# Kernel optimization log

Hardware: AMD Instinct MI355X
Metric: run time of the kernel (lower is better)

## Reference

```python
import jax, jax.numpy as jnp
import numpy as np

M = 8192      # nodes
D = 128       # feature dim
DEG = 32      # neighbors per node


def setup_inputs() -> dict:
    key = jax.random.key(0)
    ks = jax.random.split(key, 6)
    z = jax.random.normal(ks[0], (M, D), dtype=jnp.float32)
    # deterministic, duplicate-free edge list: node i -> (i+1..i+DEG) mod M
    src = jnp.repeat(jnp.arange(M, dtype=jnp.int64), DEG)
    dst = (src + jnp.tile(jnp.arange(1, DEG + 1, dtype=jnp.int64), M)) % M
    edge_index = jnp.stack([src, dst], axis=0)  # [2, M*DEG]
    s = 1.0 / np.sqrt(D)
    Wg = jax.random.normal(ks[1], (D, D), dtype=jnp.float32) * s
    Wc = jax.random.normal(ks[2], (D, D), dtype=jnp.float32) * s
    Wq = jax.random.normal(ks[3], (D, D), dtype=jnp.float32) * s
    Wk = jax.random.normal(ks[4], (D, D), dtype=jnp.float32) * s
    a = jax.random.normal(ks[5], (2 * D,), dtype=jnp.float32)
    return {"z": z, "edge_index": edge_index, "Wg": Wg, "Wc": Wc,
            "Wq": Wq, "Wk": Wk, "a": a}


def reference(z, edge_index, Wg, Wc, Wq, Wk, a):
    m, d = z.shape
    wg = z @ Wg.T                              # [m, d]
    src, dst = edge_index[0], edge_index[1]
    a_src, a_dst = a[:d], a[d:]
    # per-edge score: leaky_relu(a . [wg[i], wg[j]]) = leaky_relu(a1.wg[i] + a2.wg[j])
    scores = jax.nn.leaky_relu((wg @ a_src)[src] + (wg @ a_dst)[dst])  # [E]
    # softmax over each source node's neighbors (segment softmax)
    smax = jax.ops.segment_max(scores, src, num_segments=m)
    ex = jnp.exp(scores - smax[src])
    denom = jax.ops.segment_sum(ex, src, num_segments=m)
    alpha = ex / denom[src]                    # [E]
    # scatter-aggregate: local[i] = sum_j alpha_ij * wg[j]
    local = jax.ops.segment_sum(alpha[:, None] * wg[dst], src, num_segments=m)
    # dense global attention branch
    q = z @ Wq.T
    k = z @ Wk.T
    beta = jax.nn.softmax(q @ k.T / jnp.sqrt(jnp.float32(d)), axis=-1)  # [m, m]
    global_msg = beta @ (z @ Wc.T)
    return jax.nn.leaky_relu(local + global_msg + z)
```

## Files before the change

kernel.cpp:

```cpp
#include <hip/hip_runtime.h>

#define MM 8192
#define DD 128
#define DEG 32
#define KSPLIT 8
#define NB 16
#define RSTAGE 48

typedef __attribute__((ext_vector_type(8))) _Float16 h8;
typedef __attribute__((ext_vector_type(4))) float f4;
typedef __attribute__((ext_vector_type(4))) unsigned int u4;
typedef __attribute__((ext_vector_type(4))) short s4;

__device__ __forceinline__ unsigned short f2h(float f) {
  _Float16 h = (_Float16)f;
  return __builtin_bit_cast(unsigned short, h);
}

__device__ __forceinline__ void lds_dma16(const unsigned short* gptr, unsigned short* lptr) {
  __builtin_amdgcn_global_load_lds(
      (const __attribute__((address_space(1))) unsigned int*)gptr,
      (__attribute__((address_space(3))) unsigned int*)lptr, 16, 0, 0);
}

__global__ __launch_bounds__(256) void proj_kernel(
    const float* __restrict__ z, const float* __restrict__ Wg,
    const float* __restrict__ Wc, const float* __restrict__ Wq,
    const float* __restrict__ Wk, const float* __restrict__ a,
    float* __restrict__ wg, unsigned short* __restrict__ qb,
    unsigned short* __restrict__ kb, unsigned short* __restrict__ ct,
    float* __restrict__ sg, float* __restrict__ sd)
{
  __shared__ unsigned short zt[64 * 136];
  __shared__ unsigned short wt[128 * 136];
  const int mode = blockIdx.y;
  const float* __restrict__ W = (mode == 0) ? Wg : (mode == 1) ? Wq : (mode == 2) ? Wk : Wc;
  const int r0 = blockIdx.x * 64;
  const int tid = threadIdx.x;

  #pragma unroll
  for (int it = 0; it < 8; ++it) {
    int id = tid + it * 256, row = id >> 5, c4 = (id & 31) * 4;
    f4 v = *(const f4*)(z + (r0 + row) * DD + c4);
    s4 sv = {(short)f2h(v.x), (short)f2h(v.y), (short)f2h(v.z), (short)f2h(v.w)};
    *(s4*)&zt[row * 136 + c4] = sv;
  }
  #pragma unroll
  for (int it = 0; it < 16; ++it) {
    int id = tid + it * 256, row = id >> 5, c4 = (id & 31) * 4;
    f4 v = *(const f4*)(W + row * DD + c4);
    s4 sv = {(short)f2h(v.x), (short)f2h(v.y), (short)f2h(v.z), (short)f2h(v.w)};
    *(s4*)&wt[row * 136 + c4] = sv;
  }
  __syncthreads();

  const int lane = tid & 63, w = tid >> 6, n = lane & 15, quad = lane >> 4;
  h8 afr[4];
  #pragma unroll
  for (int kt = 0; kt < 4; ++kt)
    afr[kt] = *(const h8*)&zt[(16 * w + n) * 136 + kt * 32 + quad * 8];

  f4 acc[8];
  const f4 fzero = {0.f, 0.f, 0.f, 0.f};
  #pragma unroll
  for (int nt = 0; nt < 8; ++nt) {
    f4 c = fzero;
    #pragma unroll
    for (int kt = 0; kt < 4; ++kt) {
      h8 b = *(const h8*)&wt[(16 * nt + n) * 136 + kt * 32 + quad * 8];
      c = __builtin_amdgcn_mfma_f32_16x16x32_f16(afr[kt], b, c, 0, 0, 0);
    }
    acc[nt] = c;
  }

  if (mode == 0) {
    #pragma unroll
    for (int nt = 0; nt < 8; ++nt)
      #pragma unroll
      for (int r = 0; r < 4; ++r)
        wg[(r0 + 16 * w + quad * 4 + r) * DD + 16 * nt + n] = acc[nt][r];
    float av[8], bv[8];
    #pragma unroll
    for (int nt = 0; nt < 8; ++nt) { av[nt] = a[16 * nt + n]; bv[nt] = a[DD + 16 * nt + n]; }
    #pragma unroll
    for (int r = 0; r < 4; ++r) {
      float s1 = 0.f, s2 = 0.f;
      #pragma unroll
      for (int nt = 0; nt < 8; ++nt) { s1 += acc[nt][r] * av[nt]; s2 += acc[nt][r] * bv[nt]; }
      s1 += __shfl_xor(s1, 1); s1 += __shfl_xor(s1, 2); s1 += __shfl_xor(s1, 4); s1 += __shfl_xor(s1, 8);
      s2 += __shfl_xor(s2, 1); s2 += __shfl_xor(s2, 2); s2 += __shfl_xor(s2, 4); s2 += __shfl_xor(s2, 8);
      if (n == 0) {
        int g = r0 + 16 * w + quad * 4 + r;
        sg[g] = s1; sd[g] = s2;
      }
    }
  } else if (mode == 1) {
    const float qscale = 0.08838834764831845f;
    #pragma unroll
    for (int nt = 0; nt < 8; ++nt)
      #pragma unroll
      for (int r = 0; r < 4; ++r)
        qb[(r0 + 16 * w + quad * 4 + r) * DD + 16 * nt + n] = f2h(acc[nt][r] * qscale);
  } else if (mode == 2) {
    #pragma unroll
    for (int nt = 0; nt < 8; ++nt)
      #pragma unroll
      for (int r = 0; r < 4; ++r)
        kb[(r0 + 16 * w + quad * 4 + r) * DD + 16 * nt + n] = f2h(acc[nt][r]);
  } else {
    __syncthreads();
    #pragma unroll
    for (int nt = 0; nt < 8; ++nt)
      #pragma unroll
      for (int r = 0; r < 4; ++r)
        wt[(16 * nt + n) * 80 + 16 * w + quad * 4 + r] = f2h(acc[nt][r]);
    __syncthreads();
    #pragma unroll
    for (int it = 0; it < 4; ++it) {
      int idx = tid + it * 256, d = idx >> 3, c8 = (idx & 7) * 8;
      u4 v = *(const u4*)&wt[d * 80 + c8];
      *(u4*)(ct + (size_t)d * MM + r0 + c8) = v;
    }
  }
}

__global__ __launch_bounds__(256, 2) void flash_kernel(
    const unsigned short* __restrict__ qb, const unsigned short* __restrict__ kb,
    const unsigned short* __restrict__ ct, unsigned short* __restrict__ Opart,
    float* __restrict__ Lpart)
{
  __shared__ unsigned short sh[37376];
  const int bx = blockIdx.x, ck = blockIdx.y;
  const int tid = threadIdx.x, lane = tid & 63, w = tid >> 6;
  const int n = lane & 15, quad = lane >> 4;
  const int ln = n, lq = quad;
  const int qr0 = bx * 128;

  #pragma unroll
  for (int it = 0; it < 8; ++it)
    lds_dma16(qb + (qr0 + it * 16 + ln) * DD + w * 32 + lq * 8,
              &sh[(it * 256 + tid) * 8]);
  __syncthreads();
  h8 aq[2][4];
  #pragma unroll
  for (int mt = 0; mt < 2; ++mt)
    #pragma unroll
    for (int kt = 0; kt < 4; ++kt)
      aq[mt][kt] = *(const h8*)&sh[((w * 2 + mt) * 4 + kt) * 512 + lane * 8];
  __syncthreads();

  const unsigned short* kp = kb + (size_t)(ck * 1024 + 4 * ln) * DD + w * 32 + lq * 8;
  const unsigned short* vp = ct + (size_t)(16 * (w >> 1) + ln) * MM + ck * 1024 + (w & 1) * 32 + lq * 8;

  #pragma unroll
  for (int it = 0; it < 4; ++it)
    lds_dma16(kp + it * DD, &sh[(it * 256 + tid) * 8]);
  #pragma unroll
  for (int it = 0; it < 4; ++it)
    lds_dma16(vp + (size_t)it * 32 * MM, &sh[8192 + (it * 256 + tid) * 8]);

  f4 acc_o[2][8];
  const f4 fzero = {0.f, 0.f, 0.f, 0.f};
  #pragma unroll
  for (int mt = 0; mt < 2; ++mt)
    #pragma unroll
    for (int dt = 0; dt < 8; ++dt) acc_o[mt][dt] = fzero;
  float l_r[2][4] = {{0.f, 0.f, 0.f, 0.f}, {0.f, 0.f, 0.f, 0.f}};
  const int pbase = 32768 + w * 1152;

  for (int t = 0; t < 16; ++t) {
    __syncthreads();
    const int cur = (t & 1) * 16384;

    if (t < 15) {
      const int nb = ((t + 1) & 1) * 16384;
      const unsigned short* kpn = kp + (size_t)(t + 1) * 64 * DD;
      const unsigned short* vpn = vp + (t + 1) * 64;
      #pragma unroll
      for (int it = 0; it < 4; ++it)
        lds_dma16(kpn + it * DD, &sh[nb + (it * 256 + tid) * 8]);
      #pragma unroll
      for (int it = 0; it < 4; ++it)
        lds_dma16(vpn + (size_t)it * 32 * MM, &sh[nb + 8192 + (it * 256 + tid) * 8]);
    }

    f4 accs[2][4];
    #pragma unroll
    for (int mt = 0; mt < 2; ++mt)
      #pragma unroll
      for (int nt = 0; nt < 4; ++nt) accs[mt][nt] = fzero;
    #pragma unroll
    for (int nt = 0; nt < 4; ++nt) {
      #pragma unroll
      for (int kt = 0; kt < 4; ++kt) {
        h8 bk = *(const h8*)&sh[cur + nt * 2048 + kt * 512 + lane * 8];
        accs[0][nt] = __builtin_amdgcn_mfma_f32_16x16x32_f16(aq[0][kt], bk, accs[0][nt], 0, 0, 0);
        accs[1][nt] = __builtin_amdgcn_mfma_f32_16x16x32_f16(aq[1][kt], bk, accs[1][nt], 0, 0, 0);
      }
    }

    h8 ap[2][2];
    #pragma unroll
    for (int mt = 0; mt < 2; ++mt) {
      #pragma unroll
      for (int r = 0; r < 4; ++r) {
        float p0 = __expf(fminf(accs[mt][0][r], 10.f));
        float p1 = __expf(fminf(accs[mt][1][r], 10.f));
        float p2 = __expf(fminf(accs[mt][2][r], 10.f));
        float p3 = __expf(fminf(accs[mt][3][r], 10.f));
        l_r[mt][r] += p0 + p1 + p2 + p3;
        unsigned int lo = ((unsigned int)f2h(p1) << 16) | f2h(p0);
        unsigned int hi = ((unsigned int)f2h(p3) << 16) | f2h(p2);
        uint2 pv; pv.x = lo; pv.y = hi;
        *(uint2*)&sh[pbase + (quad * 4 + r) * 72 + n * 4] = pv;
      }
      ap[mt][0] = *(const h8*)&sh[pbase + n * 72 + quad * 8];
      ap[mt][1] = *(const h8*)&sh[pbase + n * 72 + 32 + quad * 8];
    }

    #pragma unroll
    for (int dt = 0; dt < 8; ++dt) {
      #pragma unroll
      for (int k2 = 0; k2 < 2; ++k2) {
        h8 bv = *(const h8*)&sh[cur + 8192 + dt * 1024 + k2 * 512 + lane * 8];
        acc_o[0][dt] = __builtin_amdgcn_mfma_f32_16x16x32_f16(ap[0][k2], bv, acc_o[0][dt], 0, 0, 0);
        acc_o[1][dt] = __builtin_amdgcn_mfma_f32_16x16x32_f16(ap[1][k2], bv, acc_o[1][dt], 0, 0, 0);
      }
    }
  }

  #pragma unroll
  for (int mt = 0; mt < 2; ++mt)
    #pragma unroll
    for (int r = 0; r < 4; ++r) {
      float lv = l_r[mt][r];
      lv += __shfl_xor(lv, 1); lv += __shfl_xor(lv, 2);
      lv += __shfl_xor(lv, 4); lv += __shfl_xor(lv, 8);
      int g = qr0 + w * 32 + mt * 16 + quad * 4 + r;
      if (n == 0) Lpart[ck * MM + g] = lv;
      #pragma unroll
      for (int dt = 0; dt < 8; ++dt)
        Opart[((size_t)ck * MM + g) * DD + 16 * dt + n] = f2h(acc_o[mt][dt][r]);
    }
}

__global__ __launch_bounds__(256) void merge_kernel(
    const int* __restrict__ ei, const float* __restrict__ wg,
    const float* __restrict__ sg, const float* __restrict__ sd,
    const unsigned short* __restrict__ Opart, const float* __restrict__ Lpart,
    const float* __restrict__ z, float* __restrict__ out)
{
  __shared__ float rows_s[RSTAGE * 132];
  __shared__ float sc_s[NB][DEG];
  __shared__ float alpha_s[NB][DEG];
  __shared__ int idx_s[NB][DEG];
  const int tid = threadIdx.x;
  const int i0 = blockIdx.x * NB;

  #pragma unroll
  for (int it = 0; it < 6; ++it) {
    int idx = tid + it * 256;
    int r = idx >> 5, c4 = (idx & 31) * 4;
    int grow = (i0 + 1 + r) & (MM - 1);
    *(f4*)&rows_s[r * 132 + c4] = *(const f4*)(wg + (size_t)grow * DD + c4);
  }
  #pragma unroll
  for (int it = 0; it < 2; ++it) {
    int e = tid + it * 256;
    int ni = e >> 5, j = e & 31;
    int i = i0 + ni;
    int dstj = ei[MM * DEG + i * DEG + j];
    float s = sg[i] + sd[dstj];
    sc_s[ni][j] = s > 0.f ? s : 0.01f * s;
    idx_s[ni][j] = (dstj - (i0 + 1)) & (MM - 1);
  }
  __syncthreads();

  if (tid < NB) {
    float mx = -1e30f;
    #pragma unroll 8
    for (int j = 0; j < DEG; ++j) mx = fmaxf(mx, sc_s[tid][j]);
    float sum = 0.f;
    #pragma unroll 8
    for (int j = 0; j < DEG; ++j) { float p = __expf(sc_s[tid][j] - mx); alpha_s[tid][j] = p; sum += p; }
    float inv = 1.f / sum;
    #pragma unroll 8
    for (int j = 0; j < DEG; ++j) alpha_s[tid][j] *= inv;
  }
  __syncthreads();

  const int ni = tid >> 4, d0 = (tid & 15) * 8;
  const int i = i0 + ni;
  float acc[8] = {0.f, 0.f, 0.f, 0.f, 0.f, 0.f, 0.f, 0.f};
  #pragma unroll 4
  for (int j = 0; j < DEG; ++j) {
    float al = alpha_s[ni][j];
    int r = idx_s[ni][j];
    if (r < RSTAGE) {
      const float* src = &rows_s[r * 132 + d0];
      #pragma unroll
      for (int q = 0; q < 8; ++q) acc[q] += al * src[q];
    } else {
      const float* src = wg + (size_t)((i0 + 1 + r) & (MM - 1)) * DD + d0;
      #pragma unroll
      for (int q = 0; q < 8; ++q) acc[q] += al * src[q];
    }
  }

  float l = 0.f;
  float o[8] = {0.f, 0.f, 0.f, 0.f, 0.f, 0.f, 0.f, 0.f};
  #pragma unroll
  for (int ck = 0; ck < KSPLIT; ++ck) {
    l += Lpart[ck * MM + i];
    h8 v = *(const h8*)(Opart + ((size_t)ck * MM + i) * DD + d0);
    #pragma unroll
    for (int q = 0; q < 8; ++q) o[q] += (float)v[q];
  }
  float inv = 1.0f / l;
  const float* zp = z + (size_t)i * DD + d0;
  float* op = out + (size_t)i * DD + d0;
  #pragma unroll
  for (int q = 0; q < 8; ++q) {
    float r = o[q] * inv + acc[q] + zp[q];
    op[q] = r > 0.f ? r : 0.01f * r;
  }
}

extern "C" void kernel_launch(void* const* d_in, const int* in_sizes, int n_in,
                              void* d_out, int out_size, void* d_ws, size_t ws_size,
                              hipStream_t stream) {
  const float* z  = (const float*)d_in[0];
  const int*   ei = (const int*)d_in[1];
  const float* Wg = (const float*)d_in[2];
  const float* Wc = (const float*)d_in[3];
  const float* Wq = (const float*)d_in[4];
  const float* Wk = (const float*)d_in[5];
  const float* a  = (const float*)d_in[6];
  float* out = (float*)d_out;
  char* ws = (char*)d_ws;

  float*          wg    = (float*)(ws + 0);
  unsigned short* qb    = (unsigned short*)(ws + (4 << 20));
  unsigned short* kb    = (unsigned short*)(ws + (6 << 20));
  unsigned short* ct    = (unsigned short*)(ws + (8 << 20));
  float*          sg    = (float*)(ws + (10 << 20));
  float*          sd    = (float*)(ws + (10 << 20) + (64 << 10));
  unsigned short* Opart = (unsigned short*)(ws + (15 << 20));
  float*          Lpart = (float*)(ws + (31 << 20));

  proj_kernel<<<dim3(128, 4), 256, 0, stream>>>(z, Wg, Wc, Wq, Wk, a, wg, qb, kb, ct, sg, sd);
  flash_kernel<<<dim3(64, KSPLIT), 256, 0, stream>>>(qb, kb, ct, Opart, Lpart);
  merge_kernel<<<512, 256, 0, stream>>>(ei, wg, sg, sd, Opart, Lpart, z, out);
}
```

Measured before the change: 126.0 us.

## Double flash query tile per block, load Q directly, use exp2 with prescaled queries

The flash attention kernel now processes 256 query rows per block (64 per wave) instead of 128, so each K/V tile staged in LDS feeds twice as many MFMAs. Q fragments are loaded straight from global memory into registers rather than staged through LDS. The softmax exponent uses the hardware exp2 with log2(e) folded into the query scale. The costs are higher register pressure, occupancy cut to one block per SM, half as many blocks in the grid (256), and an explicit vmcnt wait added before each barrier.

```diff
diff --git a/kernel.cpp b/kernel.cpp
--- a/kernel.cpp
+++ b/kernel.cpp
@@ -15,6 +15,10 @@
 __device__ __forceinline__ unsigned short f2h(float f) {
   _Float16 h = (_Float16)f;
   return __builtin_bit_cast(unsigned short, h);
+}
+
+__device__ __forceinline__ float fast_exp2(float x) {
+  return __builtin_amdgcn_exp2f(x);
 }
 
 __device__ __forceinline__ void lds_dma16(const unsigned short* gptr, unsigned short* lptr) {
@@ -95,7 +99,7 @@
       }
     }
   } else if (mode == 1) {
-    const float qscale = 0.08838834764831845f;
+    const float qscale = 0.12751874963942977f;
     #pragma unroll
     for (int nt = 0; nt < 8; ++nt)
       #pragma unroll
@@ -124,30 +128,24 @@
   }
 }
 
-__global__ __launch_bounds__(256, 2) void flash_kernel(
+__global__ __launch_bounds__(256, 1) void flash_kernel(
     const unsigned short* __restrict__ qb, const unsigned short* __restrict__ kb,
     const unsigned short* __restrict__ ct, unsigned short* __restrict__ Opart,
     float* __restrict__ Lpart)
 {
-  __shared__ unsigned short sh[37376];
+  __shared__ unsigned short sh[51200];
   const int bx = blockIdx.x, ck = blockIdx.y;
   const int tid = threadIdx.x, lane = tid & 63, w = tid >> 6;
   const int n = lane & 15, quad = lane >> 4;
   const int ln = n, lq = quad;
-  const int qr0 = bx * 128;
-
-  #pragma unroll
-  for (int it = 0; it < 8; ++it)
-    lds_dma16(qb + (qr0 + it * 16 + ln) * DD + w * 32 + lq * 8,
-              &sh[(it * 256 + tid) * 8]);
-  __syncthreads();
-  h8 aq[2][4];
-  #pragma unroll
-  for (int mt = 0; mt < 2; ++mt)
+  const int qr0 = bx * 256;
+
+  h8 aq[4][4];
+  #pragma unroll
+  for (int mt = 0; mt < 4; ++mt)
     #pragma unroll
     for (int kt = 0; kt < 4; ++kt)
-      aq[mt][kt] = *(const h8*)&sh[((w * 2 + mt) * 4 + kt) * 512 + lane * 8];
-  __syncthreads();
+      aq[mt][kt] = *(const h8*)(qb + (qr0 + 64 * w + 16 * mt + n) * DD + kt * 32 + quad * 8);
 
   const unsigned short* kp = kb + (size_t)(ck * 1024 + 4 * ln) * DD + w * 32 + lq * 8;
   const unsigned short* vp = ct + (size_t)(16 * (w >> 1) + ln) * MM + ck * 1024 + (w & 1) * 32 + lq * 8;
@@ -157,23 +155,28 @@
     lds_dma16(kp + it * DD, &sh[(it * 256 + tid) * 8]);
   #pragma unroll
   for (int it = 0; it < 4; ++it)
-    lds_dma16(vp + (size_t)it * 32 * MM, &sh[8192 + (it * 256 + tid) * 8]);
-
-  f4 acc_o[2][8];
+    lds_dma16(vp + (size_t)it * 32 * MM, &sh[16384 + (it * 256 + tid) * 8]);
+
+  f4 acc_o[4][8];
   const f4 fzero = {0.f, 0.f, 0.f, 0.f};
   #pragma unroll
-  for (int mt = 0; mt < 2; ++mt)
+  for (int mt = 0; mt < 4; ++mt)
     #pragma unroll
     for (int dt = 0; dt < 8; ++dt) acc_o[mt][dt] = fzero;
-  float l_r[2][4] = {{0.f, 0.f, 0.f, 0.f}, {0.f, 0.f, 0.f, 0.f}};
-  const int pbase = 32768 + w * 1152;
+  float l_r[4][4];
+  #pragma unroll
+  for (int mt = 0; mt < 4; ++mt)
+    #pragma unroll
+    for (int r = 0; r < 4; ++r) l_r[mt][r] = 0.f;
+  const int pbase = 32768 + w * 4608;
 
   for (int t = 0; t < 16; ++t) {
+    asm volatile("s_waitcnt vmcnt(0)" ::: "memory");
     __syncthreads();
-    const int cur = (t & 1) * 16384;
+    const int cur = (t & 1) * 8192;
 
     if (t < 15) {
-      const int nb = ((t + 1) & 1) * 16384;
+      const int nb = ((t + 1) & 1) * 8192;
       const unsigned short* kpn = kp + (size_t)(t + 1) * 64 * DD;
       const unsigned short* vpn = vp + (t + 1) * 64;
       #pragma unroll
@@ -181,12 +184,12 @@
         lds_dma16(kpn + it * DD, &sh[nb + (it * 256 + tid) * 8]);
       #pragma unroll
       for (int it = 0; it < 4; ++it)
-        lds_dma16(vpn + (size_t)it * 32 * MM, &sh[nb + 8192 + (it * 256 + tid) * 8]);
-    }
-
-    f4 accs[2][4];
-    #pragma unroll
-    for (int mt = 0; mt < 2; ++mt)
+        lds_dma16(vpn + (size_t)it * 32 * MM, &sh[16384 + nb + (it * 256 + tid) * 8]);
+    }
+
+    f4 accs[4][4];
+    #pragma unroll
+    for (int mt = 0; mt < 4; ++mt)
       #pragma unroll
       for (int nt = 0; nt < 4; ++nt) accs[mt][nt] = fzero;
     #pragma unroll
@@ -194,49 +197,51 @@
       #pragma unroll
       for (int kt = 0; kt < 4; ++kt) {
         h8 bk = *(const h8*)&sh[cur + nt * 2048 + kt * 512 + lane * 8];
-        accs[0][nt] = __builtin_amdgcn_mfma_f32_16x16x32_f16(aq[0][kt], bk, accs[0][nt], 0, 0, 0);
-        accs[1][nt] = __builtin_amdgcn_mfma_f32_16x16x32_f16(aq[1][kt], bk, accs[1][nt], 0, 0, 0);
+        #pragma unroll
+        for (int mt = 0; mt < 4; ++mt)
+          accs[mt][nt] = __builtin_amdgcn_mfma_f32_16x16x32_f16(aq[mt][kt], bk, accs[mt][nt], 0, 0, 0);
       }
     }
 
-    h8 ap[2][2];
-    #pragma unroll
-    for (int mt = 0; mt < 2; ++mt) {
+    h8 ap[4][2];
+    #pragma unroll
+    for (int mt = 0; mt < 4; ++mt) {
       #pragma unroll
       for (int r = 0; r < 4; ++r) {
-        float p0 = __expf(fminf(accs[mt][0][r], 10.f));
-        float p1 = __expf(fminf(accs[mt][1][r], 10.f));
-        float p2 = __expf(fminf(accs[mt][2][r], 10.f));
-        float p3 = __expf(fminf(accs[mt][3][r], 10.f));
+        float p0 = fast_exp2(fminf(accs[mt][0][r], 14.4269504f));
+        float p1 = fast_exp2(fminf(accs[mt][1][r], 14.4269504f));
+        float p2 = fast_exp2(fminf(accs[mt][2][r], 14.4269504f));
+        float p3 = fast_exp2(fminf(accs[mt][3][r], 14.4269504f));
         l_r[mt][r] += p0 + p1 + p2 + p3;
         unsigned int lo = ((unsigned int)f2h(p1) << 16) | f2h(p0);
         unsigned int hi = ((unsigned int)f2h(p3) << 16) | f2h(p2);
         uint2 pv; pv.x = lo; pv.y = hi;
-        *(uint2*)&sh[pbase + (quad * 4 + r) * 72 + n * 4] = pv;
+        *(uint2*)&sh[pbase + (mt * 16 + quad * 4 + r) * 72 + n * 4] = pv;
       }
-      ap[mt][0] = *(const h8*)&sh[pbase + n * 72 + quad * 8];
-      ap[mt][1] = *(const h8*)&sh[pbase + n * 72 + 32 + quad * 8];
+      ap[mt][0] = *(const h8*)&sh[pbase + (mt * 16 + n) * 72 + quad * 8];
+      ap[mt][1] = *(const h8*)&sh[pbase + (mt * 16 + n) * 72 + 32 + quad * 8];
     }
 
     #pragma unroll
     for (int dt = 0; dt < 8; ++dt) {
       #pragma unroll
       for (int k2 = 0; k2 < 2; ++k2) {
-        h8 bv = *(const h8*)&sh[cur + 8192 + dt * 1024 + k2 * 512 + lane * 8];
-        acc_o[0][dt] = __builtin_amdgcn_mfma_f32_16x16x32_f16(ap[0][k2], bv, acc_o[0][dt], 0, 0, 0);
-        acc_o[1][dt] = __builtin_amdgcn_mfma_f32_16x16x32_f16(ap[1][k2], bv, acc_o[1][dt], 0, 0, 0);
+        h8 bv = *(const h8*)&sh[cur + 16384 + dt * 1024 + k2 * 512 + lane * 8];
+        #pragma unroll
+        for (int mt = 0; mt < 4; ++mt)
+          acc_o[mt][dt] = __builtin_amdgcn_mfma_f32_16x16x32_f16(ap[mt][k2], bv, acc_o[mt][dt], 0, 0, 0);
       }
     }
   }
 
   #pragma unroll
-  for (int mt = 0; mt < 2; ++mt)
+  for (int mt = 0; mt < 4; ++mt)
     #pragma unroll
     for (int r = 0; r < 4; ++r) {
       float lv = l_r[mt][r];
       lv += __shfl_xor(lv, 1); lv += __shfl_xor(lv, 2);
       lv += __shfl_xor(lv, 4); lv += __shfl_xor(lv, 8);
-      int g = qr0 + w * 32 + mt * 16 + quad * 4 + r;
+      int g = qr0 + 64 * w + 16 * mt + quad * 4 + r;
       if (n == 0) Lpart[ck * MM + g] = lv;
       #pragma unroll
       for (int dt = 0; dt < 8; ++dt)
@@ -349,6 +354,6 @@
   float*          Lpart = (float*)(ws + (31 << 20));
 
   proj_kernel<<<dim3(128, 4), 256, 0, stream>>>(z, Wg, Wc, Wq, Wk, a, wg, qb, kb, ct, sg, sd);
-  flash_kernel<<<dim3(64, KSPLIT), 256, 0, stream>>>(qb, kb, ct, Opart, Lpart);
+  flash_kernel<<<dim3(32, KSPLIT), 256, 0, stream>>>(qb, kb, ct, Opart, Lpart);
   merge_kernel<<<512, 256, 0, stream>>>(ei, wg, sg, sd, Opart, Lpart, z, out);
 }
```

After: 134.8 us. 1.07x slower.
